# Kernel optimization log

Hardware: AMD Instinct MI355X
Metric: run time of the kernel (lower is better)

The kernel has to match this reference:

```python
import jax, jax.numpy as jnp
import numpy as np

K = 5          # kernel_size per pseudo-coordinate dim
N_NODES = 50000
N_EDGES = 800000
N_GRAPHS = 128


def _spline_basis(pseudo):
    # degree-1 open B-spline basis in 2-D pseudo coordinates.
    v = jnp.clip(pseudo, 0.0, 1.0) * (K - 1)            # [E,2]
    k0 = jnp.clip(jnp.floor(v), 0, K - 2).astype(jnp.int32)  # [E,2]
    frac = v - k0.astype(v.dtype)                        # [E,2]
    return k0, frac


def _spline_conv(x, src, dst, k0, frac, weight, root, bias, n_nodes):
    # weight: [K*K, in, out]. Precompute per-node per-kernel transform
    # to avoid materializing per-edge [E,in,out] weights.
    x_k = jnp.einsum('ni,kio->nko', x, weight)           # [N, 25, out]
    out_dim = weight.shape[2]
    msg = jnp.zeros((src.shape[0], out_dim), dtype=x.dtype)
    for b0 in range(2):          # 2^dim = 4 contributing basis combos
        for b1 in range(2):
            basis = ((frac[:, 0] if b0 else 1.0 - frac[:, 0])
                     * (frac[:, 1] if b1 else 1.0 - frac[:, 1]))   # [E]
            idx = (k0[:, 0] + b0) * K + (k0[:, 1] + b1)            # [E]
            msg = msg + basis[:, None] * x_k[src, idx]             # gather [E,out]
    agg = jax.ops.segment_sum(msg, dst, num_segments=n_nodes)      # [N,out]
    deg = jax.ops.segment_sum(jnp.ones((src.shape[0],), x.dtype), dst,
                              num_segments=n_nodes)
    agg = agg / jnp.maximum(deg, 1.0)[:, None]                     # aggr='mean'
    return agg + x @ root + bias


def setup_inputs() -> dict:
    key = jax.random.key(0)
    ks = jax.random.split(key, 16)
    x = jax.random.normal(ks[0], (N_NODES, 8), dtype=jnp.float32)
    edge_index = jax.random.randint(ks[1], (2, N_EDGES), 0, N_NODES, dtype=jnp.int32)
    pseudo = jax.random.uniform(ks[2], (N_EDGES, 2), dtype=jnp.float32)
    batch = jnp.sort(jax.random.randint(ks[3], (N_NODES,), 0, N_GRAPHS, dtype=jnp.int32))
    s = 0.1
    w1 = s * jax.random.normal(ks[4], (K * K, 8, 32), dtype=jnp.float32)
    r1 = s * jax.random.normal(ks[5], (8, 32), dtype=jnp.float32)
    b1 = jnp.zeros((32,), jnp.float32)
    w2 = s * jax.random.normal(ks[6], (K * K, 32, 64), dtype=jnp.float32)
    r2 = s * jax.random.normal(ks[7], (32, 64), dtype=jnp.float32)
    b2 = jnp.zeros((64,), jnp.float32)
    w3 = s * jax.random.normal(ks[8], (K * K, 64, 64), dtype=jnp.float32)
    r3 = s * jax.random.normal(ks[9], (64, 64), dtype=jnp.float32)
    b3 = jnp.zeros((64,), jnp.float32)
    fc_w = s * jax.random.normal(ks[10], (64, 30), dtype=jnp.float32)
    fc_b = jnp.zeros((30,), jnp.float32)
    return dict(x=x, edge_index=edge_index, pseudo=pseudo, batch=batch,
                w1=w1, r1=r1, b1=b1, w2=w2, r2=r2, b2=b2, w3=w3, r3=r3, b3=b3,
                fc_w=fc_w, fc_b=fc_b)


def reference(x, edge_index, pseudo, batch, w1, r1, b1, w2, r2, b2, w3, r3, b3, fc_w, fc_b):
    src, dst = edge_index[0], edge_index[1]
    k0, frac = _spline_basis(pseudo)
    h = jax.nn.elu(_spline_conv(x, src, dst, k0, frac, w1, r1, b1, N_NODES))
    h = jax.nn.elu(_spline_conv(h, src, dst, k0, frac, w2, r2, b2, N_NODES))
    h = jax.nn.elu(_spline_conv(h, src, dst, k0, frac, w3, r3, b3, N_NODES))
    # scatter_mean pooling over graphs (data.batch)
    pooled = jax.ops.segment_sum(h, batch, num_segments=N_GRAPHS)
    cnt = jax.ops.segment_sum(jnp.ones((N_NODES,), h.dtype), batch,
                              num_segments=N_GRAPHS)
    pooled = pooled / jnp.maximum(cnt, 1.0)[:, None]     # [G,64]
    # dropout is identity at inference
    logits = pooled @ fc_w + fc_b                        # [G,30]
    return jax.nn.log_softmax(logits, axis=1)
```

## Files before the change

kernel.cpp:

```cpp
#include <hip/hip_runtime.h>
#include <hip/hip_bf16.h>
#include <math.h>


typedef __attribute__((ext_vector_type(8))) short bf16x8;
typedef __attribute__((ext_vector_type(4))) float f32x4;

constexpr int SCAN_CHUNK = 2048;

__device__ __forceinline__ unsigned short f2bf(float f) {
    union { float f; unsigned u; } v; v.f = f;
    return (unsigned short)((v.u + 0x7fffu + ((v.u >> 16) & 1u)) >> 16);
}
__device__ __forceinline__ float bf2f(unsigned short h) {
    union { unsigned u; float f; } v; v.u = ((unsigned)h) << 16;
    return v.f;
}
__device__ __forceinline__ int pairaddr(int kk) {
    int slice = kk >> 5;
    return (slice >> 1) * 72 + (slice & 1) * 32 + (kk & 31);
}


__global__ void hist_kernel(const int* __restrict__ ei, int* __restrict__ deg, int E) {
    int e = blockIdx.x * blockDim.x + threadIdx.x;
    if (e < E) atomicAdd(&deg[ei[E + e]], 1);
}

__global__ __launch_bounds__(256) void scan1_kernel(const int* __restrict__ deg,
                                                    int* __restrict__ blockSums, int n) {
    __shared__ int wsum[4];
    int tid = threadIdx.x, lane = tid & 63, wave = tid >> 6;
    int idx0 = blockIdx.x * SCAN_CHUNK + tid * 8;
    int s = 0;
    #pragma unroll
    for (int u = 0; u < 8; ++u) {
        int id = idx0 + u;
        int d = (id < n) ? deg[id] : 0;
        s += (d + 7) & ~7;
    }
    #pragma unroll
    for (int off = 1; off < 64; off <<= 1) s += __shfl_xor(s, off);
    if (lane == 0) wsum[wave] = s;
    __syncthreads();
    if (tid == 0) blockSums[blockIdx.x] = wsum[0] + wsum[1] + wsum[2] + wsum[3];
}

__global__ void scan2_kernel(int* __restrict__ blockSums, int* __restrict__ row_start,
                             int nb, int n) {
    int lane = threadIdx.x & 63;
    int v = (lane < nb) ? blockSums[lane] : 0;
    int inc = v;
    #pragma unroll
    for (int off = 1; off < 64; off <<= 1) {
        int t = __shfl_up(inc, off);
        if (lane >= off) inc += t;
    }
    if (lane < nb) blockSums[lane] = inc - v;
    if (lane == 63) row_start[n] = inc;
}

__global__ __launch_bounds__(256) void scan3_kernel(const int* __restrict__ deg,
                                                    const int* __restrict__ blockSums,
                                                    int* __restrict__ row_start,
                                                    int* __restrict__ cursor,
                                                    float* __restrict__ invdeg, int n) {
    __shared__ int wsum[4];
    int tid = threadIdx.x, lane = tid & 63, wave = tid >> 6;
    int carry = blockSums[blockIdx.x];
    int idx0 = blockIdx.x * SCAN_CHUNK + tid * 8;
    int v[8], pre[8];
    int s = 0;
    #pragma unroll
    for (int u = 0; u < 8; ++u) {
        int id = idx0 + u;
        int d = (id < n) ? deg[id] : 0;
        v[u] = d;
        pre[u] = s;
        s += (d + 7) & ~7;
    }
    int inc = s;
    #pragma unroll
    for (int off = 1; off < 64; off <<= 1) {
        int t = __shfl_up(inc, off);
        if (lane >= off) inc += t;
    }
    if (lane == 63) wsum[wave] = inc;
    __syncthreads();
    int woff = 0;
    for (int w2 = 0; w2 < wave; ++w2) woff += wsum[w2];
    int eb = carry + woff + inc - s;
    #pragma unroll
    for (int u = 0; u < 8; ++u) {
        int id = idx0 + u;
        if (id < n) {
            int rs = eb + pre[u];
            row_start[id] = rs;
            cursor[id] = rs;
            invdeg[id] = 1.0f / fmaxf((float)v[u], 1.0f);
        }
    }
}

__global__ void scatter_kernel(const int* __restrict__ ei, const float* __restrict__ pseudo,
                               const float* __restrict__ invdeg, int* __restrict__ cursor,
                               uint2* __restrict__ basisB, unsigned* __restrict__ metaB, int E) {
    int e = blockIdx.x * blockDim.x + threadIdx.x;
    if (e >= E) return;
    int src = ei[e], dst = ei[E + e];
    float p0 = pseudo[2 * e], p1 = pseudo[2 * e + 1];
    float v0 = fminf(fmaxf(p0, 0.f), 1.f) * 4.f;
    float v1 = fminf(fmaxf(p1, 0.f), 1.f) * 4.f;
    int k00 = min((int)floorf(v0), 3);
    int k01 = min((int)floorf(v1), 3);
    float f0 = v0 - (float)k00, f1 = v1 - (float)k01;
    float g0 = 1.f - f0, g1 = 1.f - f1;
    float sc = invdeg[dst];
    int i00 = k00 * 5 + k01;
    int pos = atomicAdd(&cursor[dst], 1);
    uint2 b;
    b.x = (unsigned)f2bf(g0 * g1 * sc) | ((unsigned)f2bf(g0 * f1 * sc) << 16);
    b.y = (unsigned)f2bf(f0 * g1 * sc) | ((unsigned)f2bf(f0 * f1 * sc) << 16);
    basisB[pos] = b;
    metaB[pos] = (unsigned)src | ((unsigned)i00 << 20);
}

template <int Cin, int Cout, int KW>
__global__ void wprep_kernel(const float* __restrict__ W, const float* __restrict__ root,
                             unsigned short* __restrict__ WtF) {
    constexpr int NT = Cout / 16;
    int idx = blockIdx.x * 256 + threadIdx.x;
    if (idx >= Cout * KW) return;
    int e = idx & 7;
    int lane = (idx >> 3) & 63;
    int sn = idx >> 9;
    int s = sn / NT, nt = sn - s * NT;
    int r16 = lane & 15, g8 = lane >> 4;
    int o = nt * 16 + r16;
    int kk = s * 32 + g8 * 8 + e;
    float v = 0.f;
    if (kk < 26 * Cin) {
        int k = kk / Cin, i = kk - k * Cin;
        v = (k < 25) ? W[(k * Cin + i) * Cout + o] : root[i * Cout + o];
    }
    WtF[idx] = f2bf(v);
}


template <int Cin, int Cout, bool F32IN>
__global__ __launch_bounds__(512, 4) void layer_kernel(
        const void* __restrict__ xin_, const unsigned short* __restrict__ WtF,
        const float* __restrict__ bias, const int* __restrict__ row_start,
        const int* __restrict__ row_end, const uint2* __restrict__ basisG,
        const unsigned* __restrict__ metaG, unsigned short* __restrict__ xout,
        int nNodes) {
    constexpr int T = 16;
    constexpr int SLICES = (26 * Cin + 31) / 32;
    constexpr int NPAIR = (SLICES + 1) / 2;
    constexpr int ST = NPAIR * 72 + 8;
    constexpr int MT = (Cin + 15) / 16;
    constexpr int NT_B = Cout / 16;
    constexpr int W8 = 8 / NT_B;
    constexpr int RS = Cout + 4;
    constexpr int BSZ = 32 * 34;

    __shared__ __align__(16) unsigned short acc[T * ST];
    __shared__ __align__(16) unsigned short Ball[8 * BSZ];

    const int tid = threadIdx.x;
    const int node0 = blockIdx.x * T;
    const int wave = tid >> 6, lane = tid & 63;
    const int r16 = lane & 15, g8 = lane >> 4;
    const float* xf = (const float*)xin_;
    const unsigned short* xb = (const unsigned short*)xin_;

    {
        uint4 z = make_uint4(0u, 0u, 0u, 0u);
        for (int p = tid; p < T * ST / 8; p += 512) ((uint4*)acc)[p] = z;
    }
    __syncthreads();
    for (int p = tid; p < T * Cin; p += 512) {
        int t = p / Cin, i = p - t * Cin;
        int n = node0 + t;
        if (n < nNodes) {
            unsigned short v = F32IN ? f2bf(xf[n * Cin + i]) : xb[n * Cin + i];
            acc[t * ST + pairaddr(25 * Cin + i)] = v;
        }
    }

    unsigned short* Bw = Ball + wave * BSZ;
    {
        const int t0 = wave, t1 = wave + 8;
        const int na = node0 + t0, nb = node0 + t1;
        int eb0 = 0, ee0 = 0, eb1 = 0, ee1 = 0;
        if (na < nNodes) { eb0 = row_start[na]; ee0 = row_end[na]; }
        if (nb < nNodes) { eb1 = row_start[nb]; ee1 = row_end[nb]; }
        const int nc0 = (ee0 - eb0 + 31) >> 5;
        const int nc1 = (ee1 - eb1 + 31) >> 5;
        const int TC = nc0 + nc1;

        if (TC > 0) {
            auto info = [&](int vc, int& base, int& ee) {
                bool first = vc < nc0;
                int c = first ? vc : vc - nc0;
                base = (first ? eb0 : eb1) + (c << 5);
                ee = first ? ee0 : ee1;
            };
            auto loadMeta = [&](int vc, uint4& a, uint4& b) {
                int base, ee;
                info(vc, base, ee);
                const uint4* p = (const uint4*)(metaG + base + g8 * 8);
                a = p[0];
                b = p[1];
            };
            auto gatherA = [&](const uint4& a, const uint4& b, bf16x8* af) {
                int s[8];
                s[0] = a.x & 0xFFFFF; s[1] = a.y & 0xFFFFF;
                s[2] = a.z & 0xFFFFF; s[3] = a.w & 0xFFFFF;
                s[4] = b.x & 0xFFFFF; s[5] = b.y & 0xFFFFF;
                s[6] = b.z & 0xFFFFF; s[7] = b.w & 0xFFFFF;
                #pragma unroll
                for (int mt = 0; mt < MT; ++mt) {
                    int col = (Cin >= 16) ? (mt * 16 + r16) : (r16 & (Cin - 1));
                    #pragma unroll
                    for (int j = 0; j < 8; ++j)
                        af[mt][j] = (short)(F32IN ? f2bf(xf[s[j] * Cin + col])
                                                  : xb[s[j] * Cin + col]);
                }
            };
            auto loadScat = [&](int vc, unsigned& bx, unsigned& by, int& i00,
                                bool& valid) {
                int base, ee;
                info(vc, base, ee);
                int e = base + (lane & 31);
                valid = (lane < 32) && (e < ee);
                uint2 bb = basisG[e];
                unsigned mm = metaG[e];
                bx = bb.x;
                by = bb.y;
                i00 = (int)(mm >> 20);
            };

            f32x4 d[MT][2];
            #pragma unroll
            for (int mt = 0; mt < MT; ++mt)
                #pragma unroll
                for (int nt = 0; nt < 2; ++nt)
                    d[mt][nt] = (f32x4){0.f, 0.f, 0.f, 0.f};

            auto spill = [&](int t) {
                #pragma unroll
                for (int nt = 0; nt < 2; ++nt) {
                    int k = nt * 16 + r16;
                    if (k < 25) {
                        #pragma unroll
                        for (int mt = 0; mt < MT; ++mt) {
                            int ch0 = mt * 16 + g8 * 4;
                            if (ch0 < Cin) {
                                unsigned p0 = (unsigned)f2bf(d[mt][nt][0]) |
                                              ((unsigned)f2bf(d[mt][nt][1]) << 16);
                                unsigned p1 = (unsigned)f2bf(d[mt][nt][2]) |
                                              ((unsigned)f2bf(d[mt][nt][3]) << 16);
                                *(uint2*)&acc[t * ST + pairaddr(k * Cin + ch0)] =
                                    make_uint2(p0, p1);
                            }
                        }
                    }
                }
                #pragma unroll
                for (int mt = 0; mt < MT; ++mt)
                    #pragma unroll
                    for (int nt = 0; nt < 2; ++nt)
                        d[mt][nt] = (f32x4){0.f, 0.f, 0.f, 0.f};
            };

            uint4 mA, mB, nA, nB;
            bf16x8 afC[MT], afN[MT];
            unsigned bxC, byC, bxN, byN;
            int i00C, i00N;
            bool vldC, vldN;
            loadMeta(0, mA, mB);
            gatherA(mA, mB, afC);
            loadScat(0, bxC, byC, i00C, vldC);
            loadMeta(min(1, TC - 1), nA, nB);

            for (int vc = 0; vc < TC; ++vc) {
                uint4 pA, pB;
                loadMeta(min(vc + 2, TC - 1), pA, pB);
                gatherA(nA, nB, afN);
                loadScat(min(vc + 1, TC - 1), bxN, byN, i00N, vldN);

                {
                    uint4 z = make_uint4(0u, 0u, 0u, 0u);
                    uint4* b4 = (uint4*)Bw;
                    #pragma unroll
                    for (int q = 0; q < 3; ++q) {
                        int p = lane + q * 64;
                        if (p < BSZ / 8) b4[p] = z;
                    }
                    if (vldC) {
                        int le = lane & 31;
                        Bw[le * 34 + i00C]     = (unsigned short)(bxC & 0xFFFFu);
                        Bw[le * 34 + i00C + 1] = (unsigned short)(bxC >> 16);
                        Bw[le * 34 + i00C + 5] = (unsigned short)(byC & 0xFFFFu);
                        Bw[le * 34 + i00C + 6] = (unsigned short)(byC >> 16);
                    }
                    #pragma unroll
                    for (int nt = 0; nt < 2; ++nt) {
                        bf16x8 bfr;
                        #pragma unroll
                        for (int j = 0; j < 8; ++j)
                            bfr[j] = (short)Bw[(g8 * 8 + j) * 34 + nt * 16 + r16];
                        #pragma unroll
                        for (int mt = 0; mt < MT; ++mt)
                            d[mt][nt] = __builtin_amdgcn_mfma_f32_16x16x32_bf16(
                                afC[mt], bfr, d[mt][nt], 0, 0, 0);
                    }
                }
                if (vc == nc0 - 1) spill(t0);

                #pragma unroll
                for (int mt = 0; mt < MT; ++mt) afC[mt] = afN[mt];
                bxC = bxN; byC = byN; i00C = i00N; vldC = vldN;
                nA = pA; nB = pB;
            }
            if (nc1 > 0) spill(t1);
        }
    }
    __syncthreads();

    const int q = wave / NT_B;
    const int nt = wave % NT_B;
    f32x4 db = {0.f, 0.f, 0.f, 0.f};
    {
        const unsigned short* ap = acc + r16 * ST;
        for (int s = q; s < SLICES; s += W8) {
            bf16x8 a8 = *(const bf16x8*)(ap + (s >> 1) * 72 + (s & 1) * 32 + g8 * 8);
            bf16x8 b8 = *(const bf16x8*)(WtF + ((size_t)(s * NT_B + nt) * 64 + lane) * 8);
            db = __builtin_amdgcn_mfma_f32_16x16x32_bf16(a8, b8, db, 0, 0, 0);
        }
    }
    __syncthreads();
    float* red = (float*)acc;
    if (q > 0) {
        #pragma unroll
        for (int j = 0; j < 4; ++j)
            red[((q - 1) * T + g8 * 4 + j) * RS + nt * 16 + r16] = db[j];
    }
    __syncthreads();
    if (q == 0) {
        const int o = nt * 16 + r16;
        const float bo = bias[o];
        #pragma unroll
        for (int j = 0; j < 4; ++j) {
            int row = g8 * 4 + j;
            int n = node0 + row;
            if (n < nNodes) {
                float v = db[j] + bo;
                #pragma unroll
                for (int q2 = 1; q2 < W8; ++q2)
                    v += red[((q2 - 1) * T + row) * RS + o];
                v = (v > 0.f) ? v : expm1f(v);
                xout[n * Cout + o] = f2bf(v);
            }
        }
    }
}


__global__ void pool_kernel(const unsigned short* __restrict__ h, const int* __restrict__ batch,
                            float* __restrict__ pooled, float* __restrict__ cnt, int n) {
    int gw = (blockIdx.x * blockDim.x + threadIdx.x) >> 6;
    int lane = threadIdx.x & 63;
    int nw = (gridDim.x * blockDim.x) >> 6;
    int per = (n + nw - 1) / nw;
    int n0 = gw * per, n1 = min(n0 + per, n);
    if (n0 >= n1) return;
    int cur = batch[n0];
    float s = 0.f, c = 0.f;
    for (int nn = n0; nn < n1; ++nn) {
        int g = batch[nn];
        if (g != cur) {
            atomicAdd(&pooled[cur * 64 + lane], s);
            if (lane == 0) atomicAdd(&cnt[cur], c);
            s = 0.f; c = 0.f; cur = g;
        }
        s += bf2f(h[nn * 64 + lane]);
        c += 1.f;
    }
    atomicAdd(&pooled[cur * 64 + lane], s);
    if (lane == 0) atomicAdd(&cnt[cur], c);
}

__global__ __launch_bounds__(128) void head_kernel(const float* __restrict__ pooled,
                                                   const float* __restrict__ cnt,
                                                   const float* __restrict__ fcw,
                                                   const float* __restrict__ fcb,
                                                   float* __restrict__ outp, int G) {
    int g = threadIdx.x;
    if (g >= G) return;
    float inv = 1.f / fmaxf(cnt[g], 1.f);
    float l[30];
    float m = -1e30f;
    #pragma unroll
    for (int j = 0; j < 30; ++j) {
        float s = fcb[j];
        for (int i = 0; i < 64; ++i) s += pooled[g * 64 + i] * inv * fcw[i * 30 + j];
        l[j] = s;
        m = fmaxf(m, s);
    }
    float lse = 0.f;
    #pragma unroll
    for (int j = 0; j < 30; ++j) lse += expf(l[j] - m);
    lse = logf(lse);
    #pragma unroll
    for (int j = 0; j < 30; ++j) outp[g * 30 + j] = l[j] - m - lse;
}


extern "C" void kernel_launch(void* const* d_in, const int* in_sizes, int n_in,
                              void* d_out, int out_size, void* d_ws, size_t ws_size,
                              hipStream_t stream) {
    const float* x = (const float*)d_in[0];
    const int* ei = (const int*)d_in[1];
    const float* ps = (const float*)d_in[2];
    const int* batch = (const int*)d_in[3];
    const float *w1 = (const float*)d_in[4], *r1 = (const float*)d_in[5], *b1 = (const float*)d_in[6];
    const float *w2 = (const float*)d_in[7], *r2 = (const float*)d_in[8], *b2 = (const float*)d_in[9];
    const float *w3 = (const float*)d_in[10], *r3 = (const float*)d_in[11], *b3 = (const float*)d_in[12];
    const float *fcw = (const float*)d_in[13], *fcb = (const float*)d_in[14];
    float* outp = (float*)d_out;

    const int nN = in_sizes[0] / 8;
    const int E = in_sizes[1] / 2;
    const int G = out_size / 30;
    const int EP = E + 8 * nN + 64;
    const int NSB = (nN + SCAN_CHUNK - 1) / SCAN_CHUNK;

    char* wsb = (char*)d_ws;
    size_t off = 0;
    auto alloc = [&](size_t b) -> char* {
        char* p = wsb + off;
        off = (off + b + 255) & ~(size_t)255;
        return p;
    };
    int* deg = (int*)alloc((size_t)nN * 4);
    int* row_start = (int*)alloc((size_t)(nN + 1) * 4);
    int* cursor = (int*)alloc((size_t)nN * 4);
    float* invdeg = (float*)alloc((size_t)nN * 4);
    int* blockSums = (int*)alloc((size_t)64 * 4);
    uint2* basisB = (uint2*)alloc((size_t)EP * 8);
    unsigned* metaB = (unsigned*)alloc((size_t)EP * 4);
    unsigned short* wt1 = (unsigned short*)alloc((size_t)32 * 224 * 2);
    unsigned short* wt2 = (unsigned short*)alloc((size_t)64 * 832 * 2);
    unsigned short* wt3 = (unsigned short*)alloc((size_t)64 * 1664 * 2);
    unsigned short* h1 = (unsigned short*)alloc((size_t)nN * 32 * 2);
    unsigned short* h2 = (unsigned short*)alloc((size_t)nN * 64 * 2);
    unsigned short* h3 = (unsigned short*)alloc((size_t)nN * 64 * 2);
    float* pooled = (float*)alloc((size_t)G * 64 * 4);
    float* cnt = (float*)alloc((size_t)G * 4);
    (void)ws_size;

    hipMemsetAsync(deg, 0, (size_t)nN * 4, stream);
    hipMemsetAsync(metaB, 0, (size_t)EP * 4, stream);
    hipMemsetAsync(pooled, 0, (size_t)G * 64 * 4, stream);
    hipMemsetAsync(cnt, 0, (size_t)G * 4, stream);

    int ebk = (E + 255) / 256;
    hist_kernel<<<ebk, 256, 0, stream>>>(ei, deg, E);
    scan1_kernel<<<NSB, 256, 0, stream>>>(deg, blockSums, nN);
    scan2_kernel<<<1, 64, 0, stream>>>(blockSums, row_start, NSB, nN);
    scan3_kernel<<<NSB, 256, 0, stream>>>(deg, blockSums, row_start, cursor, invdeg, nN);
    scatter_kernel<<<ebk, 256, 0, stream>>>(ei, ps, invdeg, cursor, basisB, metaB, E);
    wprep_kernel<8, 32, 224><<<(32 * 224 + 255) / 256, 256, 0, stream>>>(w1, r1, wt1);
    wprep_kernel<32, 64, 832><<<(64 * 832 + 255) / 256, 256, 0, stream>>>(w2, r2, wt2);
    wprep_kernel<64, 64, 1664><<<(64 * 1664 + 255) / 256, 256, 0, stream>>>(w3, r3, wt3);

    int nb = (nN + 15) / 16;
    layer_kernel<8, 32, true><<<nb, 512, 0, stream>>>(
        x, wt1, b1, row_start, cursor, basisB, metaB, h1, nN);
    layer_kernel<32, 64, false><<<nb, 512, 0, stream>>>(
        h1, wt2, b2, row_start, cursor, basisB, metaB, h2, nN);
    layer_kernel<64, 64, false><<<nb, 512, 0, stream>>>(
        h2, wt3, b3, row_start, cursor, basisB, metaB, h3, nN);

    pool_kernel<<<128, 256, 0, stream>>>(h3, batch, pooled, cnt, nN);
    head_kernel<<<1, 128, 0, stream>>>(pooled, cnt, fcw, fcb, outp, G);
}
```

Before: 374.8 us.

## Use 1024-thread blocks covering 32 nodes in layers 2 and 3

The layer kernel now takes the block size as a template parameter, and the node tile scales with the wave count. Layers 2 and 3 run with 1024 threads and 32 nodes per block. In the dense MFMA phase each wave loads one weight fragment from global memory and reuses it across two 16-row M-tiles, which halves global weight traffic per node. In exchange the larger tile roughly doubles LDS use per block to about 150KB for layer 3, so only one block fits per CU. The launch bound with 1024 threads may also tighten the register budget, and block-wide barriers now span twice as many waves.

After: 398.0 us. 1.06x slower.

```diff
diff --git a/kernel.cpp b/kernel.cpp
--- a/kernel.cpp
+++ b/kernel.cpp
@@ -147,25 +147,29 @@
 }
 
 
-template <int Cin, int Cout, bool F32IN>
-__global__ __launch_bounds__(512, 4) void layer_kernel(
+template <int Cin, int Cout, int BLOCK, bool F32IN>
+__global__ __launch_bounds__(BLOCK, 4) void layer_kernel(
         const void* __restrict__ xin_, const unsigned short* __restrict__ WtF,
         const float* __restrict__ bias, const int* __restrict__ row_start,
         const int* __restrict__ row_end, const uint2* __restrict__ basisG,
         const unsigned* __restrict__ metaG, unsigned short* __restrict__ xout,
         int nNodes) {
-    constexpr int T = 16;
+    constexpr int WAVES = BLOCK / 64;
+    constexpr int T = 2 * WAVES;
+    constexpr int MTB = T / 16;
     constexpr int SLICES = (26 * Cin + 31) / 32;
     constexpr int NPAIR = (SLICES + 1) / 2;
     constexpr int ST = NPAIR * 72 + 8;
     constexpr int MT = (Cin + 15) / 16;
     constexpr int NT_B = Cout / 16;
-    constexpr int W8 = 8 / NT_B;
+    constexpr int QW = WAVES / NT_B;
+    static_assert(QW * NT_B == WAVES, "wave mapping");
     constexpr int RS = Cout + 4;
     constexpr int BSZ = 32 * 34;
+    static_assert((QW - 1) * T * RS * 4 <= T * ST * 2, "red fits in acc");
 
     __shared__ __align__(16) unsigned short acc[T * ST];
-    __shared__ __align__(16) unsigned short Ball[8 * BSZ];
+    __shared__ __align__(16) unsigned short Ball[WAVES * BSZ];
 
     const int tid = threadIdx.x;
     const int node0 = blockIdx.x * T;
@@ -176,10 +180,10 @@
 
     {
         uint4 z = make_uint4(0u, 0u, 0u, 0u);
-        for (int p = tid; p < T * ST / 8; p += 512) ((uint4*)acc)[p] = z;
+        for (int p = tid; p < T * ST / 8; p += BLOCK) ((uint4*)acc)[p] = z;
     }
     __syncthreads();
-    for (int p = tid; p < T * Cin; p += 512) {
+    for (int p = tid; p < T * Cin; p += BLOCK) {
         int t = p / Cin, i = p - t * Cin;
         int n = node0 + t;
         if (n < nNodes) {
@@ -190,7 +194,7 @@
 
     unsigned short* Bw = Ball + wave * BSZ;
     {
-        const int t0 = wave, t1 = wave + 8;
+        const int t0 = wave, t1 = wave + WAVES;
         const int na = node0 + t0, nb = node0 + t1;
         int eb0 = 0, ee0 = 0, eb1 = 0, ee1 = 0;
         if (na < nNodes) { eb0 = row_start[na]; ee0 = row_end[na]; }
@@ -331,37 +335,47 @@
 
     const int q = wave / NT_B;
     const int nt = wave % NT_B;
-    f32x4 db = {0.f, 0.f, 0.f, 0.f};
+    f32x4 db[MTB];
+    #pragma unroll
+    for (int m = 0; m < MTB; ++m) db[m] = (f32x4){0.f, 0.f, 0.f, 0.f};
     {
-        const unsigned short* ap = acc + r16 * ST;
-        for (int s = q; s < SLICES; s += W8) {
-            bf16x8 a8 = *(const bf16x8*)(ap + (s >> 1) * 72 + (s & 1) * 32 + g8 * 8);
+        for (int s = q; s < SLICES; s += QW) {
             bf16x8 b8 = *(const bf16x8*)(WtF + ((size_t)(s * NT_B + nt) * 64 + lane) * 8);
-            db = __builtin_amdgcn_mfma_f32_16x16x32_bf16(a8, b8, db, 0, 0, 0);
+            int aoff = (s >> 1) * 72 + (s & 1) * 32 + g8 * 8;
+            #pragma unroll
+            for (int m = 0; m < MTB; ++m) {
+                bf16x8 a8 = *(const bf16x8*)(acc + (m * 16 + r16) * ST + aoff);
+                db[m] = __builtin_amdgcn_mfma_f32_16x16x32_bf16(a8, b8, db[m], 0, 0, 0);
+            }
         }
     }
     __syncthreads();
     float* red = (float*)acc;
     if (q > 0) {
         #pragma unroll
-        for (int j = 0; j < 4; ++j)
-            red[((q - 1) * T + g8 * 4 + j) * RS + nt * 16 + r16] = db[j];
+        for (int m = 0; m < MTB; ++m)
+            #pragma unroll
+            for (int j = 0; j < 4; ++j)
+                red[((q - 1) * T + m * 16 + g8 * 4 + j) * RS + nt * 16 + r16] = db[m][j];
     }
     __syncthreads();
     if (q == 0) {
         const int o = nt * 16 + r16;
         const float bo = bias[o];
         #pragma unroll
-        for (int j = 0; j < 4; ++j) {
-            int row = g8 * 4 + j;
-            int n = node0 + row;
-            if (n < nNodes) {
-                float v = db[j] + bo;
-                #pragma unroll
-                for (int q2 = 1; q2 < W8; ++q2)
-                    v += red[((q2 - 1) * T + row) * RS + o];
-                v = (v > 0.f) ? v : expm1f(v);
-                xout[n * Cout + o] = f2bf(v);
+        for (int m = 0; m < MTB; ++m) {
+            #pragma unroll
+            for (int j = 0; j < 4; ++j) {
+                int row = m * 16 + g8 * 4 + j;
+                int n = node0 + row;
+                if (n < nNodes) {
+                    float v = db[m][j] + bo;
+                    #pragma unroll
+                    for (int q2 = 1; q2 < QW; ++q2)
+                        v += red[((q2 - 1) * T + row) * RS + o];
+                    v = (v > 0.f) ? v : expm1f(v);
+                    xout[n * Cout + o] = f2bf(v);
+                }
             }
         }
     }
@@ -476,12 +490,11 @@
     wprep_kernel<32, 64, 832><<<(64 * 832 + 255) / 256, 256, 0, stream>>>(w2, r2, wt2);
     wprep_kernel<64, 64, 1664><<<(64 * 1664 + 255) / 256, 256, 0, stream>>>(w3, r3, wt3);
 
-    int nb = (nN + 15) / 16;
-    layer_kernel<8, 32, true><<<nb, 512, 0, stream>>>(
+    layer_kernel<8, 32, 512, true><<<(nN + 15) / 16, 512, 0, stream>>>(
         x, wt1, b1, row_start, cursor, basisB, metaB, h1, nN);
-    layer_kernel<32, 64, false><<<nb, 512, 0, stream>>>(
+    layer_kernel<32, 64, 1024, false><<<(nN + 31) / 32, 1024, 0, stream>>>(
         h1, wt2, b2, row_start, cursor, basisB, metaB, h2, nN);
-    layer_kernel<64, 64, false><<<nb, 512, 0, stream>>>(
+    layer_kernel<64, 64, 1024, false><<<(nN + 31) / 32, 1024, 0, stream>>>(
         h2, wt3, b3, row_start, cursor, basisB, metaB, h3, nN);
 
     pool_kernel<<<128, 256, 0, stream>>>(h3, batch, pooled, cnt, nN);
```

## Gather neighbor features into LDS via direct global-to-LDS loads for wide layers

Applied to the files above, without the earlier changes.

For layers with bf16 input and at least 32 channels, neighbor rows are now fetched with 16-byte global_load_lds instructions into a per-wave LDS staging buffer. Each wave then reads its MFMA A fragments from LDS, replacing per-element scattered 2-byte global gathers. The next chunk's load is issued after the current fragments are read, so it overlaps with the MFMA and spill work. This adds LDS usage, which may lower occupancy, and a full vmcnt(0) wait at the top of every chunk that can stall on the in-flight loads.

New measurement: 409.3 us. 9.2% more time.

```diff
diff --git a/kernel.cpp b/kernel.cpp
--- a/kernel.cpp
+++ b/kernel.cpp
@@ -19,6 +19,11 @@
 __device__ __forceinline__ int pairaddr(int kk) {
     int slice = kk >> 5;
     return (slice >> 1) * 72 + (slice & 1) * 32 + (kk & 31);
+}
+__device__ __forceinline__ void gload_lds16(const void* g, void* l) {
+    __builtin_amdgcn_global_load_lds(
+        (const __attribute__((address_space(1))) unsigned int*)g,
+        (__attribute__((address_space(3))) unsigned int*)l, 16, 0, 0);
 }
 
 
@@ -155,6 +160,7 @@
         const unsigned* __restrict__ metaG, unsigned short* __restrict__ xout,
         int nNodes) {
     constexpr int T = 16;
+    constexpr bool DENSE = (Cin >= 32) && !F32IN;
     constexpr int SLICES = (26 * Cin + 31) / 32;
     constexpr int NPAIR = (SLICES + 1) / 2;
     constexpr int ST = NPAIR * 72 + 8;
@@ -163,9 +169,13 @@
     constexpr int W8 = 8 / NT_B;
     constexpr int RS = Cout + 4;
     constexpr int BSZ = 32 * 34;
+    constexpr int QI = DENSE ? (Cin / 16) : 1;
+    constexpr int EPI = 32 / QI;
+    constexpr int LPE = 64 / EPI;
 
     __shared__ __align__(16) unsigned short acc[T * ST];
     __shared__ __align__(16) unsigned short Ball[8 * BSZ];
+    __shared__ __align__(16) unsigned short Xall[DENSE ? 8 * 32 * Cin : 8];
 
     const int tid = threadIdx.x;
     const int node0 = blockIdx.x * T;
@@ -205,28 +215,6 @@
                 int c = first ? vc : vc - nc0;
                 base = (first ? eb0 : eb1) + (c << 5);
                 ee = first ? ee0 : ee1;
-            };
-            auto loadMeta = [&](int vc, uint4& a, uint4& b) {
-                int base, ee;
-                info(vc, base, ee);
-                const uint4* p = (const uint4*)(metaG + base + g8 * 8);
-                a = p[0];
-                b = p[1];
-            };
-            auto gatherA = [&](const uint4& a, const uint4& b, bf16x8* af) {
-                int s[8];
-                s[0] = a.x & 0xFFFFF; s[1] = a.y & 0xFFFFF;
-                s[2] = a.z & 0xFFFFF; s[3] = a.w & 0xFFFFF;
-                s[4] = b.x & 0xFFFFF; s[5] = b.y & 0xFFFFF;
-                s[6] = b.z & 0xFFFFF; s[7] = b.w & 0xFFFFF;
-                #pragma unroll
-                for (int mt = 0; mt < MT; ++mt) {
-                    int col = (Cin >= 16) ? (mt * 16 + r16) : (r16 & (Cin - 1));
-                    #pragma unroll
-                    for (int j = 0; j < 8; ++j)
-                        af[mt][j] = (short)(F32IN ? f2bf(xf[s[j] * Cin + col])
-                                                  : xb[s[j] * Cin + col]);
-                }
             };
             auto loadScat = [&](int vc, unsigned& bx, unsigned& by, int& i00,
                                 bool& valid) {
@@ -274,57 +262,139 @@
                         d[mt][nt] = (f32x4){0.f, 0.f, 0.f, 0.f};
             };
 
-            uint4 mA, mB, nA, nB;
-            bf16x8 afC[MT], afN[MT];
-            unsigned bxC, byC, bxN, byN;
-            int i00C, i00N;
-            bool vldC, vldN;
-            loadMeta(0, mA, mB);
-            gatherA(mA, mB, afC);
-            loadScat(0, bxC, byC, i00C, vldC);
-            loadMeta(min(1, TC - 1), nA, nB);
-
-            for (int vc = 0; vc < TC; ++vc) {
-                uint4 pA, pB;
-                loadMeta(min(vc + 2, TC - 1), pA, pB);
-                gatherA(nA, nB, afN);
-                loadScat(min(vc + 1, TC - 1), bxN, byN, i00N, vldN);
-
-                {
-                    uint4 z = make_uint4(0u, 0u, 0u, 0u);
-                    uint4* b4 = (uint4*)Bw;
-                    #pragma unroll
-                    for (int q = 0; q < 3; ++q) {
-                        int p = lane + q * 64;
-                        if (p < BSZ / 8) b4[p] = z;
+            auto computeB = [&](unsigned bxC, unsigned byC, int i00C, bool vldC,
+                                bf16x8* af) {
+                uint4 z = make_uint4(0u, 0u, 0u, 0u);
+                uint4* b4 = (uint4*)Bw;
+                #pragma unroll
+                for (int q = 0; q < 3; ++q) {
+                    int p = lane + q * 64;
+                    if (p < BSZ / 8) b4[p] = z;
+                }
+                if (vldC) {
+                    int le = lane & 31;
+                    Bw[le * 34 + i00C]     = (unsigned short)(bxC & 0xFFFFu);
+                    Bw[le * 34 + i00C + 1] = (unsigned short)(bxC >> 16);
+                    Bw[le * 34 + i00C + 5] = (unsigned short)(byC & 0xFFFFu);
+                    Bw[le * 34 + i00C + 6] = (unsigned short)(byC >> 16);
+                }
+                #pragma unroll
+                for (int nt = 0; nt < 2; ++nt) {
+                    bf16x8 bfr;
+                    #pragma unroll
+                    for (int j = 0; j < 8; ++j)
+                        bfr[j] = (short)Bw[(g8 * 8 + j) * 34 + nt * 16 + r16];
+                    #pragma unroll
+                    for (int mt = 0; mt < MT; ++mt)
+                        d[mt][nt] = __builtin_amdgcn_mfma_f32_16x16x32_bf16(
+                            af[mt], bfr, d[mt][nt], 0, 0, 0);
+                }
+            };
+
+            if constexpr (DENSE) {
+                unsigned short* xs = Xall + wave * (32 * Cin);
+                const int eSlot = lane / LPE;
+                const int seg = lane % LPE;
+
+                auto loadMetaLane = [&](int vc, int* m) {
+                    int base, ee;
+                    info(vc, base, ee);
+                    #pragma unroll
+                    for (int qq = 0; qq < QI; ++qq) {
+                        int e = min(base + qq * EPI + eSlot, ee - 1);
+                        m[qq] = (int)(metaG[e] & 0xFFFFFu);
                     }
-                    if (vldC) {
-                        int le = lane & 31;
-                        Bw[le * 34 + i00C]     = (unsigned short)(bxC & 0xFFFFu);
-                        Bw[le * 34 + i00C + 1] = (unsigned short)(bxC >> 16);
-                        Bw[le * 34 + i00C + 5] = (unsigned short)(byC & 0xFFFFu);
-                        Bw[le * 34 + i00C + 6] = (unsigned short)(byC >> 16);
+                };
+                auto issueDense = [&](const int* m) {
+                    #pragma unroll
+                    for (int qq = 0; qq < QI; ++qq) {
+                        const unsigned short* g = xb + (size_t)m[qq] * Cin + seg * 8;
+                        gload_lds16(g, xs + qq * EPI * Cin);
                     }
-                    #pragma unroll
-                    for (int nt = 0; nt < 2; ++nt) {
-                        bf16x8 bfr;
+                };
+
+                int mNext[QI];
+                loadMetaLane(0, mNext);
+                issueDense(mNext);
+                loadMetaLane(min(1, TC - 1), mNext);
+                unsigned bxC, byC, bxN, byN;
+                int i00C, i00N;
+                bool vldC, vldN;
+                loadScat(0, bxC, byC, i00C, vldC);
+
+                for (int vc = 0; vc < TC; ++vc) {
+                    asm volatile("s_waitcnt vmcnt(0)" ::: "memory");
+                    __builtin_amdgcn_sched_barrier(0);
+                    bf16x8 af[MT];
+                    #pragma unroll
+                    for (int mt = 0; mt < MT; ++mt)
                         #pragma unroll
                         for (int j = 0; j < 8; ++j)
-                            bfr[j] = (short)Bw[(g8 * 8 + j) * 34 + nt * 16 + r16];
+                            af[mt][j] = (short)xs[(g8 * 8 + j) * Cin + mt * 16 + r16];
+                    __builtin_amdgcn_sched_barrier(0);
+                    if (vc + 1 < TC) issueDense(mNext);
+                    int mTmp[QI];
+                    loadMetaLane(min(vc + 2, TC - 1), mTmp);
+                    loadScat(min(vc + 1, TC - 1), bxN, byN, i00N, vldN);
+
+                    computeB(bxC, byC, i00C, vldC, af);
+                    if (vc == nc0 - 1) spill(t0);
+
+                    #pragma unroll
+                    for (int qq = 0; qq < QI; ++qq) mNext[qq] = mTmp[qq];
+                    bxC = bxN; byC = byN; i00C = i00N; vldC = vldN;
+                }
+                if (nc1 > 0) spill(t1);
+            } else {
+                auto loadMeta = [&](int vc, uint4& a, uint4& b) {
+                    int base, ee;
+                    info(vc, base, ee);
+                    const uint4* p = (const uint4*)(metaG + base + g8 * 8);
+                    a = p[0];
+                    b = p[1];
+                };
+                auto gatherA = [&](const uint4& a, const uint4& b, bf16x8* af) {
+                    int s[8];
+                    s[0] = a.x & 0xFFFFF; s[1] = a.y & 0xFFFFF;
+                    s[2] = a.z & 0xFFFFF; s[3] = a.w & 0xFFFFF;
+                    s[4] = b.x & 0xFFFFF; s[5] = b.y & 0xFFFFF;
+                    s[6] = b.z & 0xFFFFF; s[7] = b.w & 0xFFFFF;
+                    #pragma unroll
+                    for (int mt = 0; mt < MT; ++mt) {
+                        int col = (Cin >= 16) ? (mt * 16 + r16) : (r16 & (Cin - 1));
                         #pragma unroll
-                        for (int mt = 0; mt < MT; ++mt)
-                            d[mt][nt] = __builtin_amdgcn_mfma_f32_16x16x32_bf16(
-                                afC[mt], bfr, d[mt][nt], 0, 0, 0);
+                        for (int j = 0; j < 8; ++j)
+                            af[mt][j] = (short)(F32IN ? f2bf(xf[s[j] * Cin + col])
+                                                      : xb[s[j] * Cin + col]);
                     }
+                };
+
+                uint4 mA, mB, nA, nB;
+                bf16x8 afC[MT], afN[MT];
+                unsigned bxC, byC, bxN, byN;
+                int i00C, i00N;
+                bool vldC, vldN;
+                loadMeta(0, mA, mB);
+                gatherA(mA, mB, afC);
+                loadScat(0, bxC, byC, i00C, vldC);
+                loadMeta(min(1, TC - 1), nA, nB);
+
+                for (int vc = 0; vc < TC; ++vc) {
+                    uint4 pA, pB;
+                    loadMeta(min(vc + 2, TC - 1), pA, pB);
+                    gatherA(nA, nB, afN);
+                    loadScat(min(vc + 1, TC - 1), bxN, byN, i00N, vldN);
+
+                    computeB(bxC, byC, i00C, vldC, afC);
+                    if (vc == nc0 - 1) spill(t0);
+
+                    #pragma unroll
+                    for (int mt = 0; mt < MT; ++mt) afC[mt] = afN[mt];
+                    bxC = bxN; byC = byN; i00C = i00N; vldC = vldN;
+                    nA = pA; nB = pB;
                 }
-                if (vc == nc0 - 1) spill(t0);
-
-                #pragma unroll
-                for (int mt = 0; mt < MT; ++mt) afC[mt] = afN[mt];
-                bxC = bxN; byC = byN; i00C = i00N; vldC = vldN;
-                nA = pA; nB = pB;
+                if (nc1 > 0) spill(t1);
             }
-            if (nc1 > 0) spill(t1);
         }
     }
     __syncthreads();
```
